# Kernel optimization log

Measured on AMD Instinct MI355X. Metric: run time of the kernel, lower is better.

Reference implementation:

```python
import jax, jax.numpy as jnp
import numpy as np

B, C, H, W = 16, 64, 64, 64
C1, C2 = 8, 32  # block_channels_1 = C/8, block_channels_2 = C/2


def _conv1x1(x, w, b):
    # x: [B,C,H,W], w: [O,C] (1x1 kernel), b: [O]
    return jnp.einsum('bchw,oc->bohw', x, w) + b[None, :, None, None]


def _maxpool2(x):
    # MaxPool2d(kernel_size=2): window 2x2, stride 2, no padding
    return jax.lax.reduce_window(x, -jnp.inf, jax.lax.max,
                                 (1, 1, 2, 2), (1, 1, 2, 2), 'VALID')


def setup_inputs() -> dict:
    key = jax.random.key(0)
    ks = jax.random.split(key, 10)
    s = lambda fan_in: 1.0 / np.sqrt(fan_in)
    return {
        'nonlocal_input': jax.random.normal(ks[0], (B, C, H, W), jnp.float32),
        # spectral-normalized conv weights are treated as the effective (already
        # normalized) weights; 1x1 kernels stored as [out, in]
        'w_delta': jax.random.normal(ks[1], (C1, C), jnp.float32) * s(C),
        'b_delta': jax.random.normal(ks[2], (C1,), jnp.float32) * 0.01,
        'w_phi': jax.random.normal(ks[3], (C1, C), jnp.float32) * s(C),
        'b_phi': jax.random.normal(ks[4], (C1,), jnp.float32) * 0.01,
        'w_g': jax.random.normal(ks[5], (C2, C), jnp.float32) * s(C),
        'b_g': jax.random.normal(ks[6], (C2,), jnp.float32) * 0.01,
        'w_last': jax.random.normal(ks[7], (C, C2), jnp.float32) * s(C2),
        'b_last': jax.random.normal(ks[8], (C,), jnp.float32) * 0.01,
        # torch init is zeros; use a nonzero value so the attention path matters
        'gamma': jnp.asarray([0.7], jnp.float32),
    }


def reference(nonlocal_input, w_delta, b_delta, w_phi, b_phi, w_g, b_g,
              w_last, b_last, gamma):
    x = nonlocal_input
    b, c, h, w = x.shape

    # delta: [B,C1,H,W] -> [B, HW, C1]
    delta = _conv1x1(x, w_delta, b_delta)
    delta = jnp.transpose(delta, (0, 2, 3, 1)).reshape(b, h * w, C1)

    # phi: conv + pool -> [B,C1,H/2,W/2]; NOTE: the original permutes
    # (1,0,2,3) BEFORE reshaping to [B, C1, HW/4] (faithful to source).
    phi = _maxpool2(_conv1x1(x, w_phi, b_phi))
    phi = jnp.transpose(phi, (1, 0, 2, 3)).reshape(b, C1, -1)

    # attention: [B, HW, HW/4]
    attn = jax.nn.softmax(jnp.einsum('bnk,bkm->bnm', delta, phi), axis=-1)

    # g: conv + pool -> [B, HW/4, C2]
    g = _maxpool2(_conv1x1(x, w_g, b_g))
    g = jnp.transpose(g, (0, 2, 3, 1)).reshape(b, -1, C2)

    out = jnp.einsum('bnm,bmc->bnc', attn, g)          # [B, HW, C2]
    out = out.reshape(b, h, w, C2).transpose(0, 3, 1, 2)  # [B, C2, H, W]

    return gamma[0] * _conv1x1(out, w_last, b_last) + x
```

## Files before the change

kernel.cpp:

```cpp
#include <hip/hip_runtime.h>
#include <hip/hip_bf16.h>
#include <math.h>

typedef __attribute__((ext_vector_type(8))) short bf16x8;
typedef __attribute__((ext_vector_type(4))) float f32x4;

#define B_   16
#define C_   64
#define C1_  8
#define C2_  32
#define HW_  4096
#define M_   1024
#define LOG2E 1.4426950408889634f
#define MFMA_BF16 __builtin_amdgcn_mfma_f32_16x16x32_bf16

__device__ __forceinline__ unsigned short f2bf(float f) {
  union { float f; unsigned u; } v; v.f = f;
  unsigned r = (v.u + 0x7fffu + ((v.u >> 16) & 1u)) >> 16;
  return (unsigned short)r;
}
__device__ __forceinline__ float bf2f(unsigned short h) {
  union { unsigned u; float f; } v; v.u = ((unsigned)h) << 16;
  return v.f;
}

__global__ __launch_bounds__(256, 4)
void k_pre(const float* __restrict__ x,
           const float* __restrict__ w_delta, const float* __restrict__ b_delta,
           const float* __restrict__ w_phi,  const float* __restrict__ b_phi,
           const float* __restrict__ w_g,    const float* __restrict__ b_g,
           unsigned short* __restrict__ delta_s,
           unsigned short* __restrict__ phi_s,
           unsigned short* __restrict__ g_t) {
  __shared__ float comb[2*64*49];
  int tid = threadIdx.x;

  int qt  = tid >> 6;
  int sub = tid & 63;
  int id  = blockIdx.x * 64 + sub;
  int pix = id & 3;
  int pm  = id >> 2;
  int b = pm >> 10;
  int m = pm & 1023;
  int py = 2*(m >> 5) + (pix >> 1);
  int px = 2*(m & 31) + (pix & 1);
  int n = py * 64 + px;

  int c0 = __builtin_amdgcn_readfirstlane(qt << 4);

  const float* xp = x + ((size_t)b*C_ + c0)*HW_ + n;
  float xv[16];
  #pragma unroll
  for (int i = 0; i < 16; ++i) xv[i] = xp[(size_t)i * HW_];

  float ad[8], ap[8], ag[32];
  #pragma unroll
  for (int o = 0; o < 8; ++o) {
    const float* wd = w_delta + o*C_ + c0;
    const float* wp = w_phi   + o*C_ + c0;
    float accd = 0.f, accp = 0.f;
    #pragma unroll
    for (int i = 0; i < 16; ++i) { accd += xv[i]*wd[i]; accp += xv[i]*wp[i]; }
    ad[o] = accd; ap[o] = accp;
  }
  #pragma unroll
  for (int o = 0; o < 32; ++o) {
    const float* wg = w_g + o*C_ + c0;
    float a = 0.f;
    #pragma unroll
    for (int i = 0; i < 16; ++i) a += xv[i]*wg[i];
    ag[o] = a;
  }

  if (qt == 1 || qt == 3) {
    float* cb = comb + (((qt >> 1)*64) + sub)*49;
    #pragma unroll
    for (int o = 0; o < 8; ++o) { cb[o] = ad[o]; cb[8+o] = ap[o]; }
    #pragma unroll
    for (int o = 0; o < 32; ++o) cb[16+o] = ag[o];
  }
  __syncthreads();
  if (qt == 0 || qt == 2) {
    const float* cb = comb + (((qt >> 1)*64) + sub)*49;
    #pragma unroll
    for (int o = 0; o < 8; ++o) { ad[o] += cb[o]; ap[o] += cb[8+o]; }
    #pragma unroll
    for (int o = 0; o < 32; ++o) ag[o] += cb[16+o];
  }
  __syncthreads();
  if (qt == 2) {
    float* cb = comb + sub*49;
    #pragma unroll
    for (int o = 0; o < 8; ++o) { cb[o] = ad[o]; cb[8+o] = ap[o]; }
    #pragma unroll
    for (int o = 0; o < 32; ++o) cb[16+o] = ag[o];
  }
  __syncthreads();
  if (qt == 0) {
    const float* cb = comb + sub*49;
    #pragma unroll
    for (int o = 0; o < 8; ++o) { ad[o] += cb[o]; ap[o] += cb[8+o]; }
    #pragma unroll
    for (int o = 0; o < 32; ++o) ag[o] += cb[16+o];

    __align__(16) unsigned short row[16];
    #pragma unroll
    for (int o = 0; o < 8; ++o) {
      float v = (ad[o] + b_delta[o]) * LOG2E;
      unsigned short hi = f2bf(v);
      row[o]   = hi;
      row[8+o] = f2bf(v - bf2f(hi));
    }
    uint4* dst = (uint4*)(delta_s + ((size_t)b*HW_ + n)*16);
    dst[0] = *(uint4*)&row[0];
    dst[1] = *(uint4*)&row[8];

    #pragma unroll
    for (int o = 0; o < 8; ++o) {
      float v = ap[o];
      v = fmaxf(v, __shfl_xor(v, 1));
      v = fmaxf(v, __shfl_xor(v, 2));
      ap[o] = v;
    }
    #pragma unroll
    for (int o = 0; o < 32; ++o) {
      float v = ag[o];
      v = fmaxf(v, __shfl_xor(v, 1));
      v = fmaxf(v, __shfl_xor(v, 2));
      ag[o] = v;
    }

    if ((sub & 3) == 0) {
      #pragma unroll
      for (int cp = 0; cp < 8; ++cp) {
        int f = cp*16 + b;
        float v = ap[cp] + b_phi[cp];
        unsigned short hi = f2bf(v);
        unsigned short* pr = phi_s + ((size_t)(f >> 3)*M_ + m)*16;
        pr[f & 7]       = hi;
        pr[8 + (f & 7)] = f2bf(v - bf2f(hi));
      }
      #pragma unroll
      for (int o = 0; o < 32; ++o)
        g_t[((size_t)b*C2_ + o)*M_ + m] = f2bf(ag[o] + b_g[o]);
    }
  }
}

__global__ __launch_bounds__(512, 4)
void k_attn(const float* __restrict__ x,
            const unsigned short* __restrict__ delta_s,
            const unsigned short* __restrict__ phi_s,
            const unsigned short* __restrict__ g_t,
            const float* __restrict__ w_last,
            const float* __restrict__ b_last,
            const float* __restrict__ gamma,
            float* __restrict__ out) {
  __shared__ __align__(16) unsigned char lds_raw[50176];
  unsigned short* phi_lds = (unsigned short*)lds_raw;
  unsigned short* g_lds   = (unsigned short*)(lds_raw + 16384);
  float* o_sh = (float*)lds_raw;
  float* cmb  = (float*)(lds_raw + 16896);

  int tid  = threadIdx.x;
  int lane = tid & 63;
  int wv   = tid >> 6;
  int rg   = wv & 3;
  int kh   = wv >> 2;
  int r    = lane & 15;
  int q    = lane >> 4;
  int bx = blockIdx.x;
  int b  = bx >> 5;
  int n0 = (bx & 31) * 128;

  bf16x8 df[2];
  #pragma unroll
  for (int t = 0; t < 2; ++t)
    df[t] = *(const bf16x8*)(delta_s +
             ((size_t)b*HW_ + n0 + rg*32 + t*16 + r)*16 + (q & 1)*8);

  int phi_off = (q >> 1) * 8;
  int key0 = (r >> 2)*8 + (r & 3);
  int key1 = key0 + 4;

  bf16x8 ones;
  #pragma unroll
  for (int i = 0; i < 8; ++i) ones[i] = (short)0x3F80;

  f32x4 acc[2][2];
  f32x4 den[2];
  f32x4 zero = {0,0,0,0};
  #pragma unroll
  for (int t = 0; t < 2; ++t) { acc[t][0] = zero; acc[t][1] = zero; den[t] = zero; }

  for (int p = 0; p < 2; ++p) {
    if (p) __syncthreads();
    {
      const uint4* psrc = (const uint4*)(phi_s + ((size_t)b*M_ + p*512)*16);
      uint4* pdst = (uint4*)phi_lds;
      #pragma unroll
      for (int u = 0; u < 2; ++u) pdst[tid + u*512] = psrc[tid + u*512];
      #pragma unroll
      for (int u = 0; u < 4; ++u) {
        int uu = tid + u*512;
        int c2 = uu >> 6, pos = uu & 63;
        *(uint4*)(g_lds + c2*520 + pos*8) =
            *(const uint4*)(g_t + ((size_t)b*C2_ + c2)*M_ + p*512 + pos*8);
      }
    }
    __syncthreads();

    #pragma unroll 2
    for (int kc = 0; kc < 256; kc += 32) {
      int kl = kh*256 + kc;
      bf16x8 aphi0 = *(const bf16x8*)(phi_lds + (size_t)(kl + key0)*16 + phi_off);
      bf16x8 aphi1 = *(const bf16x8*)(phi_lds + (size_t)(kl + key1)*16 + phi_off);
      bf16x8 bg0   = *(const bf16x8*)(g_lds + r*520        + kl + q*8);
      bf16x8 bg1   = *(const bf16x8*)(g_lds + (16 + r)*520 + kl + q*8);

      #pragma unroll
      for (int t = 0; t < 2; ++t) {
        f32x4 s0 = MFMA_BF16(aphi0, df[t], zero, 0, 0, 0);
        f32x4 s1 = MFMA_BF16(aphi1, df[t], zero, 0, 0, 0);
        union { bf16x8 v; __hip_bfloat162 h[4]; } e;
        e.h[0] = __float22bfloat162_rn(make_float2(__builtin_amdgcn_exp2f(s0[0]),
                                                   __builtin_amdgcn_exp2f(s0[1])));
        e.h[1] = __float22bfloat162_rn(make_float2(__builtin_amdgcn_exp2f(s0[2]),
                                                   __builtin_amdgcn_exp2f(s0[3])));
        e.h[2] = __float22bfloat162_rn(make_float2(__builtin_amdgcn_exp2f(s1[0]),
                                                   __builtin_amdgcn_exp2f(s1[1])));
        e.h[3] = __float22bfloat162_rn(make_float2(__builtin_amdgcn_exp2f(s1[2]),
                                                   __builtin_amdgcn_exp2f(s1[3])));
        acc[t][0] = MFMA_BF16(e.v, bg0, acc[t][0], 0, 0, 0);
        acc[t][1] = MFMA_BF16(e.v, bg1, acc[t][1], 0, 0, 0);
        den[t]    = MFMA_BF16(e.v, ones, den[t], 0, 0, 0);
      }
    }
  }

  __syncthreads();
  if (kh == 1) {
    #pragma unroll
    for (int t = 0; t < 2; ++t) {
      #pragma unroll
      for (int reg = 0; reg < 4; ++reg) {
        int row = rg*32 + t*16 + q*4 + reg;
        cmb[row*34 + r]      = acc[t][0][reg];
        cmb[row*34 + 16 + r] = acc[t][1][reg];
        if (r == 0) cmb[row*34 + 32] = den[t][reg];
      }
    }
  }
  __syncthreads();
  if (kh == 0) {
    #pragma unroll
    for (int t = 0; t < 2; ++t) {
      #pragma unroll
      for (int reg = 0; reg < 4; ++reg) {
        int row = rg*32 + t*16 + q*4 + reg;
        float o0 = acc[t][0][reg] + cmb[row*34 + r];
        float o1 = acc[t][1][reg] + cmb[row*34 + 16 + r];
        float dn = den[t][reg]    + cmb[row*34 + 32];
        float iv = __builtin_amdgcn_rcpf(dn);
        o_sh[row*33 + r]      = o0 * iv;
        o_sh[row*33 + 16 + r] = o1 * iv;
      }
    }
  }
  __syncthreads();

  int rr  = tid & 127;
  int wqu = __builtin_amdgcn_readfirstlane(tid >> 7);
  float o_reg[32];
  #pragma unroll
  for (int c = 0; c < 32; ++c) o_reg[c] = o_sh[rr*33 + c];
  float gm = gamma[0];
  for (int i = 0; i < 16; ++i) {
    int co = wqu*16 + i;
    const float* wl = w_last + co*32;
    float a = b_last[co];
    #pragma unroll
    for (int c = 0; c < 32; ++c) a += wl[c] * o_reg[c];
    size_t oi = ((size_t)b*C_ + co)*HW_ + (size_t)(n0 + rr);
    out[oi] = gm * a + x[oi];
  }
}

extern "C" void kernel_launch(void* const* d_in, const int* in_sizes, int n_in,
                              void* d_out, int out_size, void* d_ws, size_t ws_size,
                              hipStream_t stream) {
  const float* x       = (const float*)d_in[0];
  const float* w_delta = (const float*)d_in[1];
  const float* b_delta = (const float*)d_in[2];
  const float* w_phi   = (const float*)d_in[3];
  const float* b_phi   = (const float*)d_in[4];
  const float* w_g     = (const float*)d_in[5];
  const float* b_g     = (const float*)d_in[6];
  const float* w_last  = (const float*)d_in[7];
  const float* b_last  = (const float*)d_in[8];
  const float* gamma   = (const float*)d_in[9];
  float* out = (float*)d_out;

  unsigned short* ws = (unsigned short*)d_ws;
  unsigned short* delta_s = ws;
  unsigned short* phi_s   = ws + (size_t)B_*HW_*16;
  unsigned short* g_t     = phi_s + (size_t)B_*M_*16;

  hipLaunchKernelGGL(k_pre, dim3(1024), dim3(256), 0, stream,
                     x, w_delta, b_delta, w_phi, b_phi, w_g, b_g,
                     delta_s, phi_s, g_t);
  hipLaunchKernelGGL(k_attn, dim3(512), dim3(512), 0, stream,
                     x, delta_s, phi_s, g_t, w_last, b_last, gamma, out);
}
```

Measured before the change: 114.7 us.

## Compute delta projection inside attention kernel instead of staging through workspace

```diff
diff --git a/kernel.cpp b/kernel.cpp
--- a/kernel.cpp
+++ b/kernel.cpp
@@ -26,13 +26,11 @@
 
 __global__ __launch_bounds__(256, 4)
 void k_pre(const float* __restrict__ x,
-           const float* __restrict__ w_delta, const float* __restrict__ b_delta,
-           const float* __restrict__ w_phi,  const float* __restrict__ b_phi,
-           const float* __restrict__ w_g,    const float* __restrict__ b_g,
-           unsigned short* __restrict__ delta_s,
+           const float* __restrict__ w_phi, const float* __restrict__ b_phi,
+           const float* __restrict__ w_g,   const float* __restrict__ b_g,
            unsigned short* __restrict__ phi_s,
            unsigned short* __restrict__ g_t) {
-  __shared__ float comb[2*64*49];
+  __shared__ float comb[2*64*41];
   int tid = threadIdx.x;
 
   int qt  = tid >> 6;
@@ -53,15 +51,14 @@
   #pragma unroll
   for (int i = 0; i < 16; ++i) xv[i] = xp[(size_t)i * HW_];
 
-  float ad[8], ap[8], ag[32];
+  float ap[8], ag[32];
   #pragma unroll
   for (int o = 0; o < 8; ++o) {
-    const float* wd = w_delta + o*C_ + c0;
-    const float* wp = w_phi   + o*C_ + c0;
-    float accd = 0.f, accp = 0.f;
-    #pragma unroll
-    for (int i = 0; i < 16; ++i) { accd += xv[i]*wd[i]; accp += xv[i]*wp[i]; }
-    ad[o] = accd; ap[o] = accp;
+    const float* wp = w_phi + o*C_ + c0;
+    float a = 0.f;
+    #pragma unroll
+    for (int i = 0; i < 16; ++i) a += xv[i]*wp[i];
+    ap[o] = a;
   }
   #pragma unroll
   for (int o = 0; o < 32; ++o) {
@@ -73,47 +70,35 @@
   }
 
   if (qt == 1 || qt == 3) {
-    float* cb = comb + (((qt >> 1)*64) + sub)*49;
-    #pragma unroll
-    for (int o = 0; o < 8; ++o) { cb[o] = ad[o]; cb[8+o] = ap[o]; }
-    #pragma unroll
-    for (int o = 0; o < 32; ++o) cb[16+o] = ag[o];
+    float* cb = comb + (((qt >> 1)*64) + sub)*41;
+    #pragma unroll
+    for (int o = 0; o < 8; ++o) cb[o] = ap[o];
+    #pragma unroll
+    for (int o = 0; o < 32; ++o) cb[8+o] = ag[o];
   }
   __syncthreads();
   if (qt == 0 || qt == 2) {
-    const float* cb = comb + (((qt >> 1)*64) + sub)*49;
-    #pragma unroll
-    for (int o = 0; o < 8; ++o) { ad[o] += cb[o]; ap[o] += cb[8+o]; }
-    #pragma unroll
-    for (int o = 0; o < 32; ++o) ag[o] += cb[16+o];
+    const float* cb = comb + (((qt >> 1)*64) + sub)*41;
+    #pragma unroll
+    for (int o = 0; o < 8; ++o) ap[o] += cb[o];
+    #pragma unroll
+    for (int o = 0; o < 32; ++o) ag[o] += cb[8+o];
   }
   __syncthreads();
   if (qt == 2) {
-    float* cb = comb + sub*49;
-    #pragma unroll
-    for (int o = 0; o < 8; ++o) { cb[o] = ad[o]; cb[8+o] = ap[o]; }
-    #pragma unroll
-    for (int o = 0; o < 32; ++o) cb[16+o] = ag[o];
+    float* cb = comb + sub*41;
+    #pragma unroll
+    for (int o = 0; o < 8; ++o) cb[o] = ap[o];
+    #pragma unroll
+    for (int o = 0; o < 32; ++o) cb[8+o] = ag[o];
   }
   __syncthreads();
   if (qt == 0) {
-    const float* cb = comb + sub*49;
-    #pragma unroll
-    for (int o = 0; o < 8; ++o) { ad[o] += cb[o]; ap[o] += cb[8+o]; }
-    #pragma unroll
-    for (int o = 0; o < 32; ++o) ag[o] += cb[16+o];
-
-    __align__(16) unsigned short row[16];
-    #pragma unroll
-    for (int o = 0; o < 8; ++o) {
-      float v = (ad[o] + b_delta[o]) * LOG2E;
-      unsigned short hi = f2bf(v);
-      row[o]   = hi;
-      row[8+o] = f2bf(v - bf2f(hi));
-    }
-    uint4* dst = (uint4*)(delta_s + ((size_t)b*HW_ + n)*16);
-    dst[0] = *(uint4*)&row[0];
-    dst[1] = *(uint4*)&row[8];
+    const float* cb = comb + sub*41;
+    #pragma unroll
+    for (int o = 0; o < 8; ++o) ap[o] += cb[o];
+    #pragma unroll
+    for (int o = 0; o < 32; ++o) ag[o] += cb[8+o];
 
     #pragma unroll
     for (int o = 0; o < 8; ++o) {
@@ -149,7 +134,8 @@
 
 __global__ __launch_bounds__(512, 4)
 void k_attn(const float* __restrict__ x,
-            const unsigned short* __restrict__ delta_s,
+            const float* __restrict__ w_delta,
+            const float* __restrict__ b_delta,
             const unsigned short* __restrict__ phi_s,
             const unsigned short* __restrict__ g_t,
             const float* __restrict__ w_last,
@@ -157,6 +143,7 @@
             const float* __restrict__ gamma,
             float* __restrict__ out) {
   __shared__ __align__(16) unsigned char lds_raw[50176];
+  __shared__ __align__(8)  unsigned short delta_lds[128*16];
   unsigned short* phi_lds = (unsigned short*)lds_raw;
   unsigned short* g_lds   = (unsigned short*)(lds_raw + 16384);
   float* o_sh = (float*)lds_raw;
@@ -173,11 +160,32 @@
   int b  = bx >> 5;
   int n0 = (bx & 31) * 128;
 
+  {
+    int row  = tid & 127;
+    int cp2  = __builtin_amdgcn_readfirstlane(tid >> 7);
+    const float* wd0 = w_delta + (2*cp2)   * C_;
+    const float* wd1 = w_delta + (2*cp2+1) * C_;
+    const float* xr  = x + (size_t)b*C_*HW_ + n0 + row;
+    float a0 = 0.f, a1 = 0.f;
+    #pragma unroll
+    for (int c = 0; c < C_; ++c) {
+      float v = xr[(size_t)c * HW_];
+      a0 += v * wd0[c];
+      a1 += v * wd1[c];
+    }
+    a0 = (a0 + b_delta[2*cp2])   * LOG2E;
+    a1 = (a1 + b_delta[2*cp2+1]) * LOG2E;
+    unsigned short h0 = f2bf(a0), h1 = f2bf(a1);
+    unsigned short l0 = f2bf(a0 - bf2f(h0)), l1 = f2bf(a1 - bf2f(h1));
+    *(unsigned*)(delta_lds + row*16 + 2*cp2)     = (unsigned)h0 | ((unsigned)h1 << 16);
+    *(unsigned*)(delta_lds + row*16 + 8 + 2*cp2) = (unsigned)l0 | ((unsigned)l1 << 16);
+  }
+  __syncthreads();
+
   bf16x8 df[2];
   #pragma unroll
   for (int t = 0; t < 2; ++t)
-    df[t] = *(const bf16x8*)(delta_s +
-             ((size_t)b*HW_ + n0 + rg*32 + t*16 + r)*16 + (q & 1)*8);
+    df[t] = *(const bf16x8*)(delta_lds + (rg*32 + t*16 + r)*16 + (q & 1)*8);
 
   int phi_off = (q >> 1) * 8;
   int key0 = (r >> 2)*8 + (r & 3);
@@ -302,13 +310,11 @@
   float* out = (float*)d_out;
 
   unsigned short* ws = (unsigned short*)d_ws;
-  unsigned short* delta_s = ws;
-  unsigned short* phi_s   = ws + (size_t)B_*HW_*16;
-  unsigned short* g_t     = phi_s + (size_t)B_*M_*16;
+  unsigned short* phi_s = ws;
+  unsigned short* g_t   = ws + (size_t)B_*M_*16;
 
   hipLaunchKernelGGL(k_pre, dim3(1024), dim3(256), 0, stream,
-                     x, w_delta, b_delta, w_phi, b_phi, w_g, b_g,
-                     delta_s, phi_s, g_t);
+                     x, w_phi, b_phi, w_g, b_g, phi_s, g_t);
   hipLaunchKernelGGL(k_attn, dim3(512), dim3(512), 0, stream,
-                     x, delta_s, phi_s, g_t, w_last, b_last, gamma, out);
-}
+                     x, w_delta, b_delta, phi_s, g_t, w_last, b_last, gamma, out);
+}
```

Result: no change. 114.6 us, median of 2 (-0.1%).
